# Kernel optimization log

Measured on AMD Instinct MI355X. Metric: run time of the kernel, lower is better.

## Reference

```python
import jax, jax.numpy as jnp
import numpy as np

B, G = 64, 48            # events, grid side -> N = B*G*G nodes
N = B * G * G
DIMS = [128, 102, 73, 44, 16]   # channel schedule from GraphZ defaults
KERN = 3                 # GMM kernels on the conv layer
MAXV = 1.0               # Cartesian(max_value=neighbors=1)


def _build_graph():
    # 3x3 window graph (radius 1, self loops) per event, as in window_edges
    ix, iy = np.meshgrid(np.arange(G), np.arange(G), indexing='ij')
    ix, iy = ix.ravel(), iy.ravel()
    srcs, tgts = [], []
    for dx in (-1, 0, 1):
        for dy in (-1, 0, 1):
            jx, jy = ix + dx, iy + dy
            m = (jx >= 0) & (jx < G) & (jy >= 0) & (jy < G)
            srcs.append(jx[m] * G + jy[m])
            tgts.append(ix[m] * G + iy[m])
    src, tgt = np.concatenate(srcs), np.concatenate(tgts)
    base = (np.arange(B) * G * G)[:, None]
    ei = np.stack([(base + src[None]).ravel(), (base + tgt[None]).ravel()])
    pos = np.stack([np.tile(ix, B).astype(np.float32),
                    np.tile(iy, B).astype(np.float32),
                    np.repeat(np.arange(B), G * G).astype(np.float32)], axis=1)
    return ei.astype(np.int32), pos


def setup_inputs() -> dict:
    key = jax.random.key(0)
    ks = jax.random.split(key, 16)
    ei, pos = _build_graph()
    inp = {
        'x': jax.random.normal(ks[0], (N, DIMS[0]), jnp.float32),
        'pos': jnp.asarray(pos),
        'edge_index': jnp.asarray(ei),
    }
    # pointwise layer 0: 128->102 (+BN)
    inp['w0'] = jax.random.normal(ks[1], (DIMS[0], DIMS[1]), jnp.float32) * (1.0 / np.sqrt(DIMS[0]))
    inp['b0'] = jnp.zeros((DIMS[1],), jnp.float32)
    inp['gamma0'] = jnp.ones((DIMS[1],), jnp.float32)
    inp['beta0'] = jnp.zeros((DIMS[1],), jnp.float32)
    # pointwise layer 1: 102->73 (+BN)
    inp['w1'] = jax.random.normal(ks[2], (DIMS[1], DIMS[2]), jnp.float32) * (1.0 / np.sqrt(DIMS[1]))
    inp['b1'] = jnp.zeros((DIMS[2],), jnp.float32)
    inp['gamma1'] = jnp.ones((DIMS[2],), jnp.float32)
    inp['beta1'] = jnp.zeros((DIMS[2],), jnp.float32)
    # GMM conv layer 2: 73->44, 3 gaussian kernels (+BN)
    inp['w2'] = jax.random.normal(ks[3], (DIMS[2], DIMS[3]), jnp.float32) * (1.0 / np.sqrt(DIMS[2]))
    inp['g2'] = jax.random.normal(ks[4], (DIMS[2], KERN * DIMS[3]), jnp.float32) * (1.0 / np.sqrt(DIMS[2]))
    inp['mu2'] = jax.random.uniform(ks[5], (KERN, 2), jnp.float32)
    inp['sigma2'] = jax.random.uniform(ks[6], (KERN, 2), jnp.float32) + 0.5
    inp['b2'] = jnp.zeros((DIMS[3],), jnp.float32)
    inp['gamma2'] = jnp.ones((DIMS[3],), jnp.float32)
    inp['beta2'] = jnp.zeros((DIMS[3],), jnp.float32)
    # pointwise layer 3: 44->16
    inp['w3'] = jax.random.normal(ks[7], (DIMS[3], DIMS[4]), jnp.float32) * (1.0 / np.sqrt(DIMS[3]))
    inp['b3'] = jnp.zeros((DIMS[4],), jnp.float32)
    return inp


def _bn(x, gamma, beta):
    # BatchNorm1d training forward: biased batch stats over the node dim
    m = jnp.mean(x, axis=0)
    v = jnp.mean((x - m) ** 2, axis=0)
    return (x - m) * jax.lax.rsqrt(v + 1e-5) * gamma + beta


def _gmm_conv(x, ei, ea, g, mu, sigma, w_root, b, n):
    # PyG GMMConv (separate_gaussians=False, aggr='mean', root_weight, bias)
    E = ea.shape[0]
    kk = mu.shape[0]
    out = w_root.shape[1]
    xj = (x @ g)[ei[0]].reshape(E, kk, out)                 # gather transformed src feats
    gauss = jnp.exp(jnp.sum(-0.5 * (ea[:, None, :] - mu[None]) ** 2
                            / (1e-15 + sigma[None] ** 2), axis=-1))  # [E, K]
    msg = jnp.einsum('eko,ek->eo', xj, gauss)               # [E, out]
    s = jax.ops.segment_sum(msg, ei[1], num_segments=n)     # scatter-add to targets
    c = jax.ops.segment_sum(jnp.ones((E,), x.dtype), ei[1], num_segments=n)
    return s / jnp.maximum(c, 1.0)[:, None] + x @ w_root + b


def reference(x, pos, edge_index, w0, b0, gamma0, beta0, w1, b1, gamma1, beta1,
              w2, g2, mu2, sigma2, b2, gamma2, beta2, w3, b3):
    n = x.shape[0]
    pos2 = pos[:, :2]
    # Cartesian(max_value=1, norm=True): pseudo coords in [0, 1]
    ea = (pos2[edge_index[0]] - pos2[edge_index[1]]) / (2.0 * MAXV) + 0.5
    # layers 0,1: knn_graph(k=0) -> empty edge set -> GMMConv = root Linear + bias
    h = _bn(x @ w0 + b0, gamma0, beta0)
    h = _bn(h @ w1 + b1, gamma1, beta1)
    # layer 2: window-edge GMMConv with 3 gaussian kernels
    h = _bn(_gmm_conv(h, edge_index, ea, g2, mu2, sigma2, w2, b2, n), gamma2, beta2)
    # layer 3: pointwise, no norm
    return h @ w3 + b3
```

## Files before the change

kernel.cpp:

```cpp
#include <hip/hip_runtime.h>

#define GRIDW 48
#define NNODES 147456
#define NTILES 2304
#define GB 512

typedef __attribute__((ext_vector_type(8))) short short8;
typedef __attribute__((ext_vector_type(4))) float f32x4;
typedef __attribute__((ext_vector_type(4))) unsigned short ushort4v;

__device__ inline unsigned short f2bf(float f) {
    union { float f; unsigned u; } v; v.f = f;
    unsigned r = v.u + 0x7FFFu + ((v.u >> 16) & 1u);
    return (unsigned short)(r >> 16);
}
__device__ inline float bf2f(unsigned short h) {
    union { unsigned u; float f; } v; v.u = ((unsigned)h) << 16;
    return v.f;
}

__global__ void prep(const float* __restrict__ w0, const float* __restrict__ b0,
                     const float* __restrict__ w1, const float* __restrict__ b1,
                     const float* __restrict__ g2, const float* __restrict__ w2,
                     const float* __restrict__ b2, const float* __restrict__ w3,
                     const float* __restrict__ b3,
                     unsigned short* __restrict__ wt0, unsigned short* __restrict__ wt1,
                     unsigned short* __restrict__ wt2, unsigned short* __restrict__ wt3,
                     float* __restrict__ biasf0, float* __restrict__ biasf1,
                     float* __restrict__ biasf2, float* __restrict__ biasf3,
                     float* __restrict__ statz) {
    int id = blockIdx.x * 256 + threadIdx.x;
    if (id < 14336) {
        int col = id >> 7, k = id & 127;
        wt0[id] = (col < 102) ? f2bf(w0[k * 102 + col]) : (unsigned short)0;
    } else if (id < 24576) {
        int e = id - 14336; int col = e >> 7, k = e & 127;
        wt1[e] = (col < 73 && k < 102) ? f2bf(w1[k * 73 + col]) : (unsigned short)0;
    } else if (id < 41472) {
        int e = id - 24576; int col = e / 96, k = e - (e / 96) * 96;
        unsigned short v = 0;
        if (k < 73) v = (col < 132) ? f2bf(g2[k * 132 + col]) : f2bf(w2[k * 44 + (col - 132)]);
        wt2[e] = v;
    } else if (id < 42496) {
        int e = id - 41472; int col = e >> 6, k = e & 63;
        wt3[e] = (k < 44) ? f2bf(w3[k * 16 + col]) : (unsigned short)0;
    } else if (id < 42608) { int c = id - 42496; biasf0[c] = (c < 102) ? b0[c] : 0.f; }
    else if (id < 42688) { int c = id - 42608; biasf1[c] = (c < 73) ? b1[c] : 0.f; }
    else if (id < 42864) { int c = id - 42688; biasf2[c] = (c < 132) ? 0.f : b2[c - 132]; }
    else if (id < 42880) { int c = id - 42864; biasf3[c] = b3[c]; }
    else if (id < 43264) { statz[id - 42880] = 0.f; }
}

template<int K, int KP, int MP, int MOUT, int PREVM, int BNSRC,
         bool STATS, bool OUTBF, bool ABF16>
__global__ __launch_bounds__(256) void gemm_p(
    const void* __restrict__ Ain, const unsigned short* __restrict__ WT,
    const float* __restrict__ biasf,
    const float* __restrict__ q0, const float* __restrict__ q1,
    const float* __restrict__ q2, const float* __restrict__ q3,
    float invN, void* __restrict__ Yout,
    float* __restrict__ sumO, float* __restrict__ ssO)
{
    constexpr int KS = KP + 8;
    constexpr int NCF = MP / 16;
    constexpr int UPR = ABF16 ? (K / 8) : (K / 4);
    constexpr int TOT = 64 * UPR;
    constexpr int NLD = (TOT + 255) / 256;
    __shared__ __align__(16) unsigned short As[2][64 * KS];
    __shared__ __align__(16) unsigned short Bs[MP * KS];
    __shared__ float bnA[KP], bnB[KP];

    const int tid = threadIdx.x;
    const int lane = tid & 63, wv = tid >> 6, qd = lane >> 4, lc = lane & 15;

    if (BNSRC == 1) {
        if (tid < KP) {
            float a = 0.f, b = 0.f;
            if (tid < PREVM) {
                float m = q0[tid] * invN;
                float v = q1[tid] * invN - m * m;
                float sc = q2[tid] * rsqrtf(v + 1e-5f);
                a = sc; b = q3[tid] - m * sc;
            }
            bnA[tid] = a; bnB[tid] = b;
        }
    } else if (BNSRC == 2) {
        if (tid < KP) {
            bnA[tid] = (tid < PREVM) ? q0[tid] : 0.f;
            bnB[tid] = (tid < PREVM) ? q1[tid] : 0.f;
        }
    }
    for (int g = tid; g < MP * (KP / 8); g += 256) {
        int col = g / (KP / 8), u = g - col * (KP / 8);
        *(uint4*)&Bs[col * KS + u * 8] = *(const uint4*)&WT[(size_t)col * KP + u * 8];
    }
    if constexpr (KP > K) {
        constexpr int PADU = (KP - K) / 2;
        for (int g = tid; g < 64 * PADU; g += 256) {
            int row = g / PADU, u = g - row * PADU;
            *(unsigned*)&As[0][row * KS + K + u * 2] = 0u;
            *(unsigned*)&As[1][row * KS + K + u * 2] = 0u;
        }
    }

    float bvr[NCF];
#pragma unroll
    for (int cf = 0; cf < NCF; ++cf) bvr[cf] = biasf[cf * 16 + lc];

    float cs[NCF], cq[NCF];
    if (STATS) {
#pragma unroll
        for (int cf = 0; cf < NCF; ++cf) { cs[cf] = 0.f; cq[cf] = 0.f; }
    }

    uint4 pfb[NLD];
    float4 pff[NLD];

    int t = blockIdx.x;
#pragma unroll
    for (int i = 0; i < NLD; ++i) {
        int g = tid + 256 * i;
        if (g < TOT) {
            if constexpr (ABF16)
                pfb[i] = *(const uint4*)((const unsigned short*)Ain + (size_t)t * 64 * K + g * 8);
            else
                pff[i] = *(const float4*)((const float*)Ain + (size_t)t * 64 * K + g * 4);
        }
    }
    __syncthreads();

    int buf = 0;
    for (; t < NTILES; t += GB) {
#pragma unroll
        for (int i = 0; i < NLD; ++i) {
            int g = tid + 256 * i;
            if (g < TOT) {
                int row = g / UPR, u = g - row * UPR;
                if constexpr (ABF16) {
                    uint4 w = pfb[i];
                    if (BNSRC != 0) {
                        unsigned* wp = (unsigned*)&w;
#pragma unroll
                        for (int pp = 0; pp < 4; ++pp) {
                            int kk = u * 8 + 2 * pp;
                            float lo = bf2f((unsigned short)(wp[pp] & 0xFFFFu)) * bnA[kk] + bnB[kk];
                            float hi = bf2f((unsigned short)(wp[pp] >> 16)) * bnA[kk + 1] + bnB[kk + 1];
                            wp[pp] = (unsigned)f2bf(lo) | ((unsigned)f2bf(hi) << 16);
                        }
                    }
                    *(uint4*)&As[buf][row * KS + u * 8] = w;
                } else {
                    float4 v = pff[i];
                    if (BNSRC != 0) {
                        int kk = u * 4;
                        v.x = v.x * bnA[kk] + bnB[kk];
                        v.y = v.y * bnA[kk + 1] + bnB[kk + 1];
                        v.z = v.z * bnA[kk + 2] + bnB[kk + 2];
                        v.w = v.w * bnA[kk + 3] + bnB[kk + 3];
                    }
                    unsigned lo = (unsigned)f2bf(v.x) | ((unsigned)f2bf(v.y) << 16);
                    unsigned hi = (unsigned)f2bf(v.z) | ((unsigned)f2bf(v.w) << 16);
                    *(uint2*)&As[buf][row * KS + u * 4] = make_uint2(lo, hi);
                }
            }
        }
        int t2 = t + GB;
        if (t2 < NTILES) {
#pragma unroll
            for (int i = 0; i < NLD; ++i) {
                int g = tid + 256 * i;
                if (g < TOT) {
                    if constexpr (ABF16)
                        pfb[i] = *(const uint4*)((const unsigned short*)Ain + (size_t)t2 * 64 * K + g * 8);
                    else
                        pff[i] = *(const float4*)((const float*)Ain + (size_t)t2 * 64 * K + g * 4);
                }
            }
        }
        __syncthreads();

        f32x4 acc[NCF];
#pragma unroll
        for (int cf = 0; cf < NCF; ++cf) acc[cf] = (f32x4){0.f, 0.f, 0.f, 0.f};
#pragma unroll
        for (int kt = 0; kt < KP / 32; ++kt) {
            const int kb = kt * 32 + qd * 8;
            short8 a = *(const short8*)&As[buf][(wv * 16 + lc) * KS + kb];
#pragma unroll
            for (int cf = 0; cf < NCF; ++cf) {
                short8 b = *(const short8*)&Bs[(cf * 16 + lc) * KS + kb];
                acc[cf] = __builtin_amdgcn_mfma_f32_16x16x32_bf16(a, b, acc[cf], 0, 0, 0);
            }
        }
#pragma unroll
        for (int cf = 0; cf < NCF; ++cf) {
            const int col = cf * 16 + lc;
            const float bv = bvr[cf];
#pragma unroll
            for (int rr = 0; rr < 4; ++rr) {
                float v = acc[cf][rr] + bv;
                int row = t * 64 + wv * 16 + qd * 4 + rr;
                if (OUTBF) ((unsigned short*)Yout)[(size_t)row * MP + col] = f2bf(v);
                else       ((float*)Yout)[(size_t)row * MP + col] = v;
                if (STATS) { cs[cf] += v; cq[cf] += v * v; }
            }
        }
        buf ^= 1;
    }

    if (STATS) {
        __syncthreads();
        float* red = (float*)As;
        float* redq = red + 4 * MP;
#pragma unroll
        for (int cf = 0; cf < NCF; ++cf) {
            float s = cs[cf], qq = cq[cf];
            s += __shfl_down(s, 32, 64); s += __shfl_down(s, 16, 64);
            qq += __shfl_down(qq, 32, 64); qq += __shfl_down(qq, 16, 64);
            if (lane < 16) {
                red[wv * MP + cf * 16 + lane] = s;
                redq[wv * MP + cf * 16 + lane] = qq;
            }
        }
        __syncthreads();
        if (tid < MOUT) {
            float s = red[tid] + red[MP + tid] + red[2 * MP + tid] + red[3 * MP + tid];
            float qq = redq[tid] + redq[MP + tid] + redq[2 * MP + tid] + redq[3 * MP + tid];
            atomicAdd(&sumO[tid], s);
            atomicAdd(&ssO[tid], qq);
        }
    }
}

__global__ __launch_bounds__(256) void gmm_stencil(
    const unsigned short* __restrict__ TR, float* __restrict__ C,
    const float* __restrict__ mu, const float* __restrict__ sigma,
    float* __restrict__ partial)
{
    __shared__ float gs[9][3];
    __shared__ float red[88];
    const int tid = threadIdx.x;
    if (tid < 88) red[tid] = 0.f;
    if (tid < 27) {
        int d = tid / 3, k = tid - (tid / 3) * 3;
        int dx = d / 3 - 1, dy = d % 3 - 1;
        float ex = 0.5f * dx + 0.5f, ey = 0.5f * dy + 0.5f;
        float mx = mu[k * 2], my = mu[k * 2 + 1];
        float sx = sigma[k * 2], sy = sigma[k * 2 + 1];
        gs[d][k] = expf(-0.5f * ((ex - mx) * (ex - mx) / (1e-15f + sx * sx) +
                                 (ey - my) * (ey - my) / (1e-15f + sy * sy)));
    }
    __syncthreads();

    const int base = blockIdx.x * 256 + tid;
    const int og = base % 11;
    const int node0 = base / 11;
    const int c0 = og * 4;

    float4 s4 = make_float4(0, 0, 0, 0), q4 = make_float4(0, 0, 0, 0);

    for (int it = 0; it < 9; ++it) {
        int node = node0 + it * 16384;
        int rem = node % (GRIDW * GRIDW);
        int ix = rem / GRIDW, iy = rem - (rem / GRIDW) * GRIDW;
        float ax = 0, ay = 0, az = 0, aw = 0;
#pragma unroll
        for (int dx = -1; dx <= 1; ++dx) {
            int jx = ix + dx;
            if (jx < 0 || jx >= GRIDW) continue;
#pragma unroll
            for (int dy = -1; dy <= 1; ++dy) {
                int jy = iy + dy;
                if (jy < 0 || jy >= GRIDW) continue;
                int d = (dx + 1) * 3 + (dy + 1);
                const unsigned short* tj = TR + (size_t)(node + dx * GRIDW + dy) * 176 + c0;
                float g0 = gs[d][0], g1 = gs[d][1], g2v = gs[d][2];
                ushort4v t0 = *(const ushort4v*)tj;
                ushort4v t1 = *(const ushort4v*)(tj + 44);
                ushort4v t2 = *(const ushort4v*)(tj + 88);
                ax += g0 * bf2f(t0.x) + g1 * bf2f(t1.x) + g2v * bf2f(t2.x);
                ay += g0 * bf2f(t0.y) + g1 * bf2f(t1.y) + g2v * bf2f(t2.y);
                az += g0 * bf2f(t0.z) + g1 * bf2f(t1.z) + g2v * bf2f(t2.z);
                aw += g0 * bf2f(t0.w) + g1 * bf2f(t1.w) + g2v * bf2f(t2.w);
            }
        }
        int cnt = ((ix > 0) + (ix < GRIDW - 1) + 1) * ((iy > 0) + (iy < GRIDW - 1) + 1);
        float inv = 1.f / (float)cnt;
        const unsigned short* rp = TR + (size_t)node * 176 + 132 + c0;
        ushort4v rv = *(const ushort4v*)rp;
        float4 o;
        o.x = ax * inv + bf2f(rv.x);
        o.y = ay * inv + bf2f(rv.y);
        o.z = az * inv + bf2f(rv.z);
        o.w = aw * inv + bf2f(rv.w);
        *(float4*)&C[(size_t)node * 44 + c0] = o;
        s4.x += o.x; s4.y += o.y; s4.z += o.z; s4.w += o.w;
        q4.x += o.x * o.x; q4.y += o.y * o.y; q4.z += o.z * o.z; q4.w += o.w * o.w;
    }
    atomicAdd(&red[c0 + 0], s4.x); atomicAdd(&red[c0 + 1], s4.y);
    atomicAdd(&red[c0 + 2], s4.z); atomicAdd(&red[c0 + 3], s4.w);
    atomicAdd(&red[44 + c0 + 0], q4.x); atomicAdd(&red[44 + c0 + 1], q4.y);
    atomicAdd(&red[44 + c0 + 2], q4.z); atomicAdd(&red[44 + c0 + 3], q4.w);
    __syncthreads();
    if (tid < 88) partial[(size_t)blockIdx.x * 88 + tid] = red[tid];
}

__global__ __launch_bounds__(704) void reduce_bn2(
    const float* __restrict__ partial, const float* __restrict__ gamma,
    const float* __restrict__ beta, float* __restrict__ a2p,
    float* __restrict__ sh2p, float invN)
{
    __shared__ float part[8][88];
    __shared__ float tot[88];
    const int tid = threadIdx.x;
    const int c = tid % 88, rg = tid / 88;
    float s = 0.f;
    for (int r = rg; r < 704; r += 8) s += partial[(size_t)r * 88 + c];
    part[rg][c] = s;
    __syncthreads();
    if (tid < 88) {
        float t = 0.f;
#pragma unroll
        for (int g = 0; g < 8; ++g) t += part[g][tid];
        tot[tid] = t;
    }
    __syncthreads();
    if (tid < 64) {
        float a = 0.f, b = 0.f;
        if (tid < 44) {
            float m = tot[tid] * invN;
            float v = tot[44 + tid] * invN - m * m;
            float sc = gamma[tid] * rsqrtf(v + 1e-5f);
            a = sc; b = beta[tid] - m * sc;
        }
        a2p[tid] = a; sh2p[tid] = b;
    }
}

extern "C" void kernel_launch(void* const* d_in, const int* in_sizes, int n_in,
                              void* d_out, int out_size, void* d_ws, size_t ws_size,
                              hipStream_t stream) {
    const float* x      = (const float*)d_in[0];
    const float* w0     = (const float*)d_in[3];
    const float* b0     = (const float*)d_in[4];
    const float* gamma0 = (const float*)d_in[5];
    const float* beta0  = (const float*)d_in[6];
    const float* w1     = (const float*)d_in[7];
    const float* b1     = (const float*)d_in[8];
    const float* gamma1 = (const float*)d_in[9];
    const float* beta1  = (const float*)d_in[10];
    const float* w2     = (const float*)d_in[11];
    const float* g2     = (const float*)d_in[12];
    const float* mu2    = (const float*)d_in[13];
    const float* sigma2 = (const float*)d_in[14];
    const float* b2     = (const float*)d_in[15];
    const float* gamma2 = (const float*)d_in[16];
    const float* beta2  = (const float*)d_in[17];
    const float* w3     = (const float*)d_in[18];
    const float* b3     = (const float*)d_in[19];
    float* out = (float*)d_out;

    const int N = NNODES;
    const float invN = 1.0f / (float)N;

    const size_t tailOff = (size_t)N * 132;
    size_t need = (tailOff + 84096 + 64) * sizeof(float);
    if (ws_size < need) return;

    float* ws = (float*)d_ws;
    unsigned short* bufY1 = (unsigned short*)ws;
    float*          bufC  = ws;
    unsigned short* bufY0 = (unsigned short*)(ws + (size_t)N * 44);
    unsigned short* bufTR = bufY0;

    float* tail = ws + tailOff;
    float* sum0 = tail;
    float* ss0  = tail + 112;
    float* sum1 = tail + 224;
    float* ss1  = tail + 304;
    float* a2p  = tail + 384;
    float* sh2p = tail + 448;
    float* biasf0 = tail + 512;
    float* biasf1 = tail + 624;
    float* biasf2 = tail + 704;
    float* biasf3 = tail + 880;
    float* partial = tail + 896;
    unsigned short* wt0 = (unsigned short*)(tail + 62848);
    unsigned short* wt1 = wt0 + 14336;
    unsigned short* wt2 = wt1 + 10240;
    unsigned short* wt3 = wt2 + 16896;

    prep<<<169, 256, 0, stream>>>(w0, b0, w1, b1, g2, w2, b2, w3, b3,
                                  wt0, wt1, wt2, wt3,
                                  biasf0, biasf1, biasf2, biasf3, tail);

    gemm_p<128, 128, 112, 102, 0, 0, true, true, false><<<GB, 256, 0, stream>>>(
        x, wt0, biasf0, nullptr, nullptr, nullptr, nullptr, invN, bufY0, sum0, ss0);

    gemm_p<112, 128, 80, 73, 102, 1, true, true, true><<<GB, 256, 0, stream>>>(
        bufY0, wt1, biasf1, sum0, ss0, gamma0, beta0, invN, bufY1, sum1, ss1);

    gemm_p<80, 96, 176, 176, 73, 1, false, true, true><<<GB, 256, 0, stream>>>(
        bufY1, wt2, biasf2, sum1, ss1, gamma1, beta1, invN, bufTR, nullptr, nullptr);

    gmm_stencil<<<704, 256, 0, stream>>>(bufTR, bufC, mu2, sigma2, partial);
    reduce_bn2<<<1, 704, 0, stream>>>(partial, gamma2, beta2, a2p, sh2p, invN);

    gemm_p<44, 64, 16, 16, 64, 2, false, false, false><<<GB, 256, 0, stream>>>(
        bufC, wt3, biasf3, a2p, sh2p, nullptr, nullptr, invN, out, nullptr, nullptr);
}
```

Measured before the change: 288.5 us.

## Tile GMM stencil by event bands, store bf16 output, drop reduce kernel

The stencil kernel now assigns each block a contiguous 6-row band of one event, so the neighbour reads of the 3x3 window stay local to the block and should hit cache more often. It writes the conv output as padded bf16 (48 columns) instead of fp32, which halves that intermediate's traffic. BN statistics now go straight to global sums with atomics, so the separate reduce_bn2 launch is gone and the final GEMM applies BN from the raw sums through its BNSRC=1 path. In exchange there are more global atomics, bf16 rounding of the pre-BN activations, and 3 of every 256 threads sit idle.

```diff
diff --git a/kernel.cpp b/kernel.cpp
--- a/kernel.cpp
+++ b/kernel.cpp
@@ -48,7 +48,7 @@
     else if (id < 42688) { int c = id - 42608; biasf1[c] = (c < 73) ? b1[c] : 0.f; }
     else if (id < 42864) { int c = id - 42688; biasf2[c] = (c < 132) ? 0.f : b2[c - 132]; }
     else if (id < 42880) { int c = id - 42864; biasf3[c] = b3[c]; }
-    else if (id < 43264) { statz[id - 42880] = 0.f; }
+    else if (id < 43392) { statz[id - 42880] = 0.f; }
 }
 
 template<int K, int KP, int MP, int MOUT, int PREVM, int BNSRC,
@@ -233,9 +233,9 @@
 }
 
 __global__ __launch_bounds__(256) void gmm_stencil(
-    const unsigned short* __restrict__ TR, float* __restrict__ C,
+    const unsigned short* __restrict__ TR, unsigned short* __restrict__ C,
     const float* __restrict__ mu, const float* __restrict__ sigma,
-    float* __restrict__ partial)
+    float* __restrict__ sum2, float* __restrict__ ss2)
 {
     __shared__ float gs[9][3];
     __shared__ float red[88];
@@ -252,89 +252,69 @@
     }
     __syncthreads();
 
-    const int base = blockIdx.x * 256 + tid;
-    const int og = base % 11;
-    const int node0 = base / 11;
-    const int c0 = og * 4;
-
-    float4 s4 = make_float4(0, 0, 0, 0), q4 = make_float4(0, 0, 0, 0);
-
-    for (int it = 0; it < 9; ++it) {
-        int node = node0 + it * 16384;
-        int rem = node % (GRIDW * GRIDW);
-        int ix = rem / GRIDW, iy = rem - (rem / GRIDW) * GRIDW;
-        float ax = 0, ay = 0, az = 0, aw = 0;
-#pragma unroll
-        for (int dx = -1; dx <= 1; ++dx) {
-            int jx = ix + dx;
-            if (jx < 0 || jx >= GRIDW) continue;
-#pragma unroll
-            for (int dy = -1; dy <= 1; ++dy) {
-                int jy = iy + dy;
-                if (jy < 0 || jy >= GRIDW) continue;
-                int d = (dx + 1) * 3 + (dy + 1);
-                const unsigned short* tj = TR + (size_t)(node + dx * GRIDW + dy) * 176 + c0;
-                float g0 = gs[d][0], g1 = gs[d][1], g2v = gs[d][2];
-                ushort4v t0 = *(const ushort4v*)tj;
-                ushort4v t1 = *(const ushort4v*)(tj + 44);
-                ushort4v t2 = *(const ushort4v*)(tj + 88);
-                ax += g0 * bf2f(t0.x) + g1 * bf2f(t1.x) + g2v * bf2f(t2.x);
-                ay += g0 * bf2f(t0.y) + g1 * bf2f(t1.y) + g2v * bf2f(t2.y);
-                az += g0 * bf2f(t0.z) + g1 * bf2f(t1.z) + g2v * bf2f(t2.z);
-                aw += g0 * bf2f(t0.w) + g1 * bf2f(t1.w) + g2v * bf2f(t2.w);
-            }
-        }
-        int cnt = ((ix > 0) + (ix < GRIDW - 1) + 1) * ((iy > 0) + (iy < GRIDW - 1) + 1);
-        float inv = 1.f / (float)cnt;
-        const unsigned short* rp = TR + (size_t)node * 176 + 132 + c0;
-        ushort4v rv = *(const ushort4v*)rp;
-        float4 o;
-        o.x = ax * inv + bf2f(rv.x);
-        o.y = ay * inv + bf2f(rv.y);
-        o.z = az * inv + bf2f(rv.z);
-        o.w = aw * inv + bf2f(rv.w);
-        *(float4*)&C[(size_t)node * 44 + c0] = o;
-        s4.x += o.x; s4.y += o.y; s4.z += o.z; s4.w += o.w;
-        q4.x += o.x * o.x; q4.y += o.y * o.y; q4.z += o.z * o.z; q4.w += o.w * o.w;
-    }
-    atomicAdd(&red[c0 + 0], s4.x); atomicAdd(&red[c0 + 1], s4.y);
-    atomicAdd(&red[c0 + 2], s4.z); atomicAdd(&red[c0 + 3], s4.w);
-    atomicAdd(&red[44 + c0 + 0], q4.x); atomicAdd(&red[44 + c0 + 1], q4.y);
-    atomicAdd(&red[44 + c0 + 2], q4.z); atomicAdd(&red[44 + c0 + 3], q4.w);
+    const int r = blockIdx.x & 7;
+    const int m = blockIdx.x >> 3;
+    const int batch = r * 8 + (m >> 3);
+    const int band = m & 7;
+    const int base = batch * 2304 + band * 288;
+
+    if (tid < 253) {
+        const int og = tid % 11;
+        const int ln0 = tid / 11;
+        const int c0 = og * 4;
+        float4 s4 = make_float4(0, 0, 0, 0), q4 = make_float4(0, 0, 0, 0);
+
+        for (int i = 0; i < 13; ++i) {
+            int ln = ln0 + 23 * i;
+            if (ln >= 288) break;
+            int node = base + ln;
+            int rx = ln / 48, iy = ln - rx * 48;
+            int ix = band * 6 + rx;
+            float ax = 0, ay = 0, az = 0, aw = 0;
+#pragma unroll
+            for (int dx = -1; dx <= 1; ++dx) {
+                int jx = ix + dx;
+                if (jx < 0 || jx >= GRIDW) continue;
+#pragma unroll
+                for (int dy = -1; dy <= 1; ++dy) {
+                    int jy = iy + dy;
+                    if (jy < 0 || jy >= GRIDW) continue;
+                    int d = (dx + 1) * 3 + (dy + 1);
+                    const unsigned short* tj = TR + (size_t)(node + dx * GRIDW + dy) * 176 + c0;
+                    float g0 = gs[d][0], g1 = gs[d][1], g2v = gs[d][2];
+                    ushort4v t0 = *(const ushort4v*)tj;
+                    ushort4v t1 = *(const ushort4v*)(tj + 44);
+                    ushort4v t2 = *(const ushort4v*)(tj + 88);
+                    ax += g0 * bf2f(t0.x) + g1 * bf2f(t1.x) + g2v * bf2f(t2.x);
+                    ay += g0 * bf2f(t0.y) + g1 * bf2f(t1.y) + g2v * bf2f(t2.y);
+                    az += g0 * bf2f(t0.z) + g1 * bf2f(t1.z) + g2v * bf2f(t2.z);
+                    aw += g0 * bf2f(t0.w) + g1 * bf2f(t1.w) + g2v * bf2f(t2.w);
+                }
+            }
+            int cnt = ((ix > 0) + (ix < GRIDW - 1) + 1) * ((iy > 0) + (iy < GRIDW - 1) + 1);
+            float inv = 1.f / (float)cnt;
+            const unsigned short* rp = TR + (size_t)node * 176 + 132 + c0;
+            ushort4v rv = *(const ushort4v*)rp;
+            float ox = ax * inv + bf2f(rv.x);
+            float oy = ay * inv + bf2f(rv.y);
+            float oz = az * inv + bf2f(rv.z);
+            float ow = aw * inv + bf2f(rv.w);
+            unsigned lo = (unsigned)f2bf(ox) | ((unsigned)f2bf(oy) << 16);
+            unsigned hi = (unsigned)f2bf(oz) | ((unsigned)f2bf(ow) << 16);
+            *(uint2*)&C[(size_t)node * 48 + c0] = make_uint2(lo, hi);
+            if (og == 10)
+                *(uint2*)&C[(size_t)node * 48 + 44] = make_uint2(0u, 0u);
+            s4.x += ox; s4.y += oy; s4.z += oz; s4.w += ow;
+            q4.x += ox * ox; q4.y += oy * oy; q4.z += oz * oz; q4.w += ow * ow;
+        }
+        atomicAdd(&red[c0 + 0], s4.x); atomicAdd(&red[c0 + 1], s4.y);
+        atomicAdd(&red[c0 + 2], s4.z); atomicAdd(&red[c0 + 3], s4.w);
+        atomicAdd(&red[44 + c0 + 0], q4.x); atomicAdd(&red[44 + c0 + 1], q4.y);
+        atomicAdd(&red[44 + c0 + 2], q4.z); atomicAdd(&red[44 + c0 + 3], q4.w);
+    }
     __syncthreads();
-    if (tid < 88) partial[(size_t)blockIdx.x * 88 + tid] = red[tid];
-}
-
-__global__ __launch_bounds__(704) void reduce_bn2(
-    const float* __restrict__ partial, const float* __restrict__ gamma,
-    const float* __restrict__ beta, float* __restrict__ a2p,
-    float* __restrict__ sh2p, float invN)
-{
-    __shared__ float part[8][88];
-    __shared__ float tot[88];
-    const int tid = threadIdx.x;
-    const int c = tid % 88, rg = tid / 88;
-    float s = 0.f;
-    for (int r = rg; r < 704; r += 8) s += partial[(size_t)r * 88 + c];
-    part[rg][c] = s;
-    __syncthreads();
-    if (tid < 88) {
-        float t = 0.f;
-#pragma unroll
-        for (int g = 0; g < 8; ++g) t += part[g][tid];
-        tot[tid] = t;
-    }
-    __syncthreads();
-    if (tid < 64) {
-        float a = 0.f, b = 0.f;
-        if (tid < 44) {
-            float m = tot[tid] * invN;
-            float v = tot[44 + tid] * invN - m * m;
-            float sc = gamma[tid] * rsqrtf(v + 1e-5f);
-            a = sc; b = beta[tid] - m * sc;
-        }
-        a2p[tid] = a; sh2p[tid] = b;
-    }
+    if (tid < 44) atomicAdd(&sum2[tid], red[tid]);
+    else if (tid < 88) atomicAdd(&ss2[tid - 44], red[tid]);
 }
 
 extern "C" void kernel_launch(void* const* d_in, const int* in_sizes, int n_in,
@@ -364,12 +344,12 @@
     const float invN = 1.0f / (float)N;
 
     const size_t tailOff = (size_t)N * 132;
-    size_t need = (tailOff + 84096 + 64) * sizeof(float);
+    size_t need = (tailOff + 90000) * sizeof(float);
     if (ws_size < need) return;
 
     float* ws = (float*)d_ws;
     unsigned short* bufY1 = (unsigned short*)ws;
-    float*          bufC  = ws;
+    unsigned short* bufC  = (unsigned short*)ws;
     unsigned short* bufY0 = (unsigned short*)(ws + (size_t)N * 44);
     unsigned short* bufTR = bufY0;
 
@@ -378,14 +358,13 @@
     float* ss0  = tail + 112;
     float* sum1 = tail + 224;
     float* ss1  = tail + 304;
-    float* a2p  = tail + 384;
-    float* sh2p = tail + 448;
+    float* sum2 = tail + 384;
+    float* ss2  = tail + 448;
     float* biasf0 = tail + 512;
     float* biasf1 = tail + 624;
     float* biasf2 = tail + 704;
     float* biasf3 = tail + 880;
-    float* partial = tail + 896;
-    unsigned short* wt0 = (unsigned short*)(tail + 62848);
+    unsigned short* wt0 = (unsigned short*)(tail + 896);
     unsigned short* wt1 = wt0 + 14336;
     unsigned short* wt2 = wt1 + 10240;
     unsigned short* wt3 = wt2 + 16896;
@@ -403,9 +382,8 @@
     gemm_p<80, 96, 176, 176, 73, 1, false, true, true><<<GB, 256, 0, stream>>>(
         bufY1, wt2, biasf2, sum1, ss1, gamma1, beta1, invN, bufTR, nullptr, nullptr);
 
-    gmm_stencil<<<704, 256, 0, stream>>>(bufTR, bufC, mu2, sigma2, partial);
-    reduce_bn2<<<1, 704, 0, stream>>>(partial, gamma2, beta2, a2p, sh2p, invN);
-
-    gemm_p<44, 64, 16, 16, 64, 2, false, false, false><<<GB, 256, 0, stream>>>(
-        bufC, wt3, biasf3, a2p, sh2p, nullptr, nullptr, invN, out, nullptr, nullptr);
-}
+    gmm_stencil<<<512, 256, 0, stream>>>(bufTR, bufC, mu2, sigma2, sum2, ss2);
+
+    gemm_p<48, 64, 16, 16, 44, 1, false, false, true><<<GB, 256, 0, stream>>>(
+        bufC, wt3, biasf3, sum2, ss2, gamma2, beta2, invN, out, nullptr, nullptr);
+}
```

After: 267.0 us. -7.5%, faster.
